# Kernel tuning notes

Hardware: AMD Instinct MI355X
Metric: run time of the kernel (lower is better)

The kernel has to match this reference:

```python
import jax, jax.numpy as jnp
import numpy as np

B, C, H, W = 4, 256, 64, 64
DIV = 4
D = C // DIV  # 64


def setup_inputs() -> dict:
    key = jax.random.key(0)
    ks = jax.random.split(key, 10)
    s = 0.05
    return {
        "x": jax.random.normal(ks[0], (B, C, H, W), dtype=jnp.float32),
        "wq": jax.random.normal(ks[1], (D, C), dtype=jnp.float32) * s,
        "bq": jax.random.normal(ks[2], (D,), dtype=jnp.float32) * s,
        "wk": jax.random.normal(ks[3], (D, C), dtype=jnp.float32) * s,
        "bk": jax.random.normal(ks[4], (D,), dtype=jnp.float32) * s,
        "wv": jax.random.normal(ks[5], (D, C), dtype=jnp.float32) * s,
        "bv": jax.random.normal(ks[6], (D,), dtype=jnp.float32) * s,
        "wsa": jax.random.normal(ks[7], (C, D), dtype=jnp.float32) * s,
        "bsa": jax.random.normal(ks[8], (C,), dtype=jnp.float32) * s,
        "gamma": jnp.zeros((1,), dtype=jnp.float32) + 0.5,
    }


def reference(x, wq, bq, wk, bk, wv, bv, wsa, bsa, gamma):
    b, c, h, w = x.shape
    hw = h * w
    xf = x.reshape(b, c, hw)  # [b, c, hw]
    # 1x1 convs == per-pixel linear maps
    q = jnp.einsum('dc,bcn->bdn', wq, xf) + bq[None, :, None]  # [b, d, hw]
    k = jnp.einsum('dc,bcn->bdn', wk, xf) + bk[None, :, None]
    v = jnp.einsum('dc,bcn->bdn', wv, xf) + bv[None, :, None]
    # attn[b, i, j] = softmax_j( q[:, :, i] . k[:, :, j] )
    scores = jnp.einsum('bdi,bdj->bij', q, k)  # [b, hw, hw]
    attn = jax.nn.softmax(scores, axis=-1)
    # sa = v @ attn^T : sa[b, d, i] = sum_j v[b, d, j] * attn[b, i, j]
    sa = jnp.einsum('bdj,bij->bdi', v, attn)  # [b, d, hw]
    out = jnp.einsum('cd,bdn->bcn', wsa, sa) + bsa[None, :, None]  # [b, c, hw]
    out = out.reshape(b, c, h, w)
    return gamma[0] * out + x
```

## Files before the change

kernel.cpp:

```cpp
#include <hip/hip_runtime.h>
#include <hip/hip_bf16.h>

typedef short short8 __attribute__((ext_vector_type(8)));
typedef float f32x4  __attribute__((ext_vector_type(4)));

static constexpr int NB  = 4;
static constexpr int NC  = 256;
static constexpr int NHW = 4096;
static constexpr int ND  = 64;
static constexpr int SPLIT = 8;
static constexpr int JITER = NHW / 64 / SPLIT;
static constexpr float SHIFT = 12.0f;

__device__ inline float bfbits2f(unsigned short u) {
    union { unsigned int i; float f; } x; x.i = ((unsigned int)u) << 16; return x.f;
}

__global__ __launch_bounds__(256) void wcvt_kernel(
    const float* __restrict__ wq, const float* __restrict__ wk,
    const float* __restrict__ wv, const float* __restrict__ wsa,
    __hip_bfloat16* __restrict__ wqkv_bf, __hip_bfloat16* __restrict__ wsa_bf)
{
    const int idx = blockIdx.x * 256 + threadIdx.x;
    if (idx < 192 * 256) {
        const int row = idx >> 8, col = idx & 255;
        const float* src = row < 64 ? wq : (row < 128 ? wk : wv);
        wqkv_bf[idx] = __float2bfloat16(src[(row & 63) * 256 + col]);
    } else {
        const int i = idx - 192 * 256;
        wsa_bf[i] = __float2bfloat16(wsa[i]);
    }
}

__global__ __launch_bounds__(512) void qkv_kernel(
    const float* __restrict__ x, const __hip_bfloat16* __restrict__ wqkv,
    const float* __restrict__ bq, const float* __restrict__ bk,
    const float* __restrict__ bv,
    __hip_bfloat16* __restrict__ qt, __hip_bfloat16* __restrict__ kt,
    __hip_bfloat16* __restrict__ vd)
{
    const int b  = blockIdx.x;
    const int n0 = blockIdx.y * 32;
    __shared__ __align__(16) __hip_bfloat16 xs[32][256];
    __shared__ __align__(16) __hip_bfloat16 vt_s[64][40];

    const int t  = threadIdx.x;
    const int tn = t & 31;
    const int cq = t >> 5;

    const float* xb = x + (size_t)b * NC * NHW + n0;
    #pragma unroll
    for (int kblk = 0; kblk < 4; ++kblk) {
        const int c0 = cq * 4 + kblk * 64;
        __hip_bfloat16 pk[4];
        #pragma unroll
        for (int j = 0; j < 4; ++j)
            pk[j] = __float2bfloat16(xb[(size_t)(c0 + j) * NHW + tn]);
        const int kk = (c0 >> 3) ^ (tn & 7);
        *(uint2*)&xs[tn][kk * 8 + (c0 & 7)] = *(uint2*)pk;
    }
    __syncthreads();

    const int w    = t >> 6;
    const int wm   = w >> 2;
    const int wn   = w & 3;
    const int lane = t & 63;
    const int c    = lane & 15;
    const int q    = lane >> 4;

    f32x4 acc[3];
    #pragma unroll
    for (int nt = 0; nt < 3; ++nt) acc[nt] = (f32x4){0.f, 0.f, 0.f, 0.f};

    const int row = wm * 16 + c;
    #pragma unroll
    for (int kc = 0; kc < 8; ++kc) {
        const int kk = (kc * 4 + q) ^ (row & 7);
        const short8 a = *(const short8*)&xs[row][kk * 8];
        #pragma unroll
        for (int nt = 0; nt < 3; ++nt) {
            const short8 bfr = *(const short8*)(wqkv
                + (size_t)(wn * 48 + nt * 16 + c) * 256 + kc * 32 + q * 8);
            acc[nt] = __builtin_amdgcn_mfma_f32_16x16x32_bf16(a, bfr, acc[nt], 0, 0, 0);
        }
    }

    #pragma unroll
    for (int nt = 0; nt < 3; ++nt) {
        const int j0   = wn * 48 + nt * 16;
        const int sel  = j0 >> 6;
        const int colr = (j0 & 63) + c;
        const float bias = (sel == 0 ? bq : (sel == 1 ? bk : bv))[colr];
        if (sel < 2) {
            __hip_bfloat16* dst = (sel == 0 ? qt : kt);
            #pragma unroll
            for (int r = 0; r < 4; ++r) {
                const int prow = wm * 16 + q * 4 + r;
                dst[((size_t)(b * NHW) + n0 + prow) * ND + colr] =
                    __float2bfloat16(acc[nt][r] + bias);
            }
        } else {
            #pragma unroll
            for (int r = 0; r < 4; ++r)
                vt_s[colr][wm * 16 + q * 4 + r] =
                    __float2bfloat16(acc[nt][r] + bias);
        }
    }
    __syncthreads();
    if (t < 256) {
        const int d = t >> 2, nc8 = (t & 3) * 8;
        *(short8*)(vd + ((size_t)(b * ND) + d) * NHW + n0 + nc8) =
            *(const short8*)&vt_s[d][nc8];
    }
}

__global__ __launch_bounds__(256, 4) void attn_kernel(
    const __hip_bfloat16* __restrict__ qt,
    const __hip_bfloat16* __restrict__ kt,
    const __hip_bfloat16* __restrict__ vd,
    __hip_bfloat16* __restrict__ O_part, float* __restrict__ l_part)
{
    const int b  = blockIdx.x;
    const int q0 = blockIdx.y * 128;
    const int s  = blockIdx.z;

    __shared__ __align__(16) __hip_bfloat16 ks [64][72];
    __shared__ __align__(16) __hip_bfloat16 vts[64][72];
    __shared__ __align__(16) __hip_bfloat16 ps [4][32][72];

    const int t    = threadIdx.x;
    const int w    = t >> 6;
    const int lane = t & 63;
    const int c    = lane & 15;
    const int q    = lane >> 4;

    short8 qf[2][2];
    #pragma unroll
    for (int mt = 0; mt < 2; ++mt)
        #pragma unroll
        for (int ch = 0; ch < 2; ++ch)
            qf[mt][ch] = *(const short8*)(qt
                + ((size_t)(b * NHW) + q0 + w * 32 + mt * 16 + c) * ND
                + ch * 32 + q * 8);

    f32x4 O[2][4];
    #pragma unroll
    for (int mt = 0; mt < 2; ++mt)
        #pragma unroll
        for (int dt = 0; dt < 4; ++dt)
            O[mt][dt] = (f32x4){0.f, 0.f, 0.f, 0.f};
    float lsum[2] = {0.f, 0.f};

    const int row_s = t >> 3;
    const int c8    = (t & 7) * 8;
    short8 kpre[2], vpre[2];
    {
        const int j0 = s * (NHW / SPLIT);
        kpre[0] = *(const short8*)(kt + ((size_t)(b * NHW) + j0 + row_s) * ND + c8);
        kpre[1] = *(const short8*)(kt + ((size_t)(b * NHW) + j0 + 32 + row_s) * ND + c8);
        vpre[0] = *(const short8*)(vd + ((size_t)(b * ND) + row_s) * NHW + j0 + c8);
        vpre[1] = *(const short8*)(vd + ((size_t)(b * ND) + 32 + row_s) * NHW + j0 + c8);
    }

    for (int it = 0; it < JITER; ++it) {
        __syncthreads();
        *(short8*)&ks [row_s     ][c8] = kpre[0];
        *(short8*)&ks [32 + row_s][c8] = kpre[1];
        *(short8*)&vts[row_s     ][c8] = vpre[0];
        *(short8*)&vts[32 + row_s][c8] = vpre[1];
        if (it + 1 < JITER) {
            const int j0 = s * (NHW / SPLIT) + (it + 1) * 64;
            kpre[0] = *(const short8*)(kt + ((size_t)(b * NHW) + j0 + row_s) * ND + c8);
            kpre[1] = *(const short8*)(kt + ((size_t)(b * NHW) + j0 + 32 + row_s) * ND + c8);
            vpre[0] = *(const short8*)(vd + ((size_t)(b * ND) + row_s) * NHW + j0 + c8);
            vpre[1] = *(const short8*)(vd + ((size_t)(b * ND) + 32 + row_s) * NHW + j0 + c8);
        }
        __syncthreads();

        #pragma unroll
        for (int jt = 0; jt < 4; ++jt) {
            const short8 kf0 = *(const short8*)&ks[jt * 16 + c][q * 8];
            const short8 kf1 = *(const short8*)&ks[jt * 16 + c][32 + q * 8];
            #pragma unroll
            for (int mt = 0; mt < 2; ++mt) {
                f32x4 acc = (f32x4){0.f, 0.f, 0.f, 0.f};
                acc = __builtin_amdgcn_mfma_f32_16x16x32_bf16(kf0, qf[mt][0], acc, 0, 0, 0);
                acc = __builtin_amdgcn_mfma_f32_16x16x32_bf16(kf1, qf[mt][1], acc, 0, 0, 0);
                __hip_bfloat16 pk[4];
                float ls = 0.f;
                #pragma unroll
                for (int r = 0; r < 4; ++r) {
                    const float p = __expf(acc[r] - SHIFT);
                    ls += p;
                    pk[r] = __float2bfloat16(p);
                }
                lsum[mt] += ls;
                *(uint2*)&ps[w][mt * 16 + c][jt * 16 + q * 4] = *(uint2*)pk;
            }
        }

        short8 af[2][2];
        #pragma unroll
        for (int mt = 0; mt < 2; ++mt) {
            af[mt][0] = *(const short8*)&ps[w][mt * 16 + c][q * 8];
            af[mt][1] = *(const short8*)&ps[w][mt * 16 + c][32 + q * 8];
        }
        #pragma unroll
        for (int dt = 0; dt < 4; ++dt) {
            const short8 vf0 = *(const short8*)&vts[dt * 16 + c][q * 8];
            const short8 vf1 = *(const short8*)&vts[dt * 16 + c][32 + q * 8];
            #pragma unroll
            for (int mt = 0; mt < 2; ++mt) {
                O[mt][dt] = __builtin_amdgcn_mfma_f32_16x16x32_bf16(af[mt][0], vf0, O[mt][dt], 0, 0, 0);
                O[mt][dt] = __builtin_amdgcn_mfma_f32_16x16x32_bf16(af[mt][1], vf1, O[mt][dt], 0, 0, 0);
            }
        }
    }

    const size_t sb = (size_t)(s * NB + b);
    #pragma unroll
    for (int mt = 0; mt < 2; ++mt) {
        float lv = lsum[mt];
        lv += __shfl_xor(lv, 16);
        lv += __shfl_xor(lv, 32);
        if (lane < 16)
            l_part[sb * NHW + q0 + w * 32 + mt * 16 + c] = lv;
    }
    #pragma unroll
    for (int mt = 0; mt < 2; ++mt)
        #pragma unroll
        for (int dt = 0; dt < 4; ++dt)
            #pragma unroll
            for (int r = 0; r < 4; ++r) {
                const int row = q0 + w * 32 + mt * 16 + q * 4 + r;
                O_part[(sb * NHW + row) * ND + dt * 16 + c] =
                    __float2bfloat16(O[mt][dt][r]);
            }
}

__global__ __launch_bounds__(256) void combine_kernel(
    const __hip_bfloat16* __restrict__ O_part, const float* __restrict__ l_part,
    __hip_bfloat16* __restrict__ sat)
{
    const int idx = blockIdx.x * 256 + threadIdx.x;
    const size_t bn = (size_t)(idx >> 4);
    const int d4 = (idx & 15) * 4;
    float num[4] = {0.f, 0.f, 0.f, 0.f};
    float den = 0.f;
    #pragma unroll
    for (int s = 0; s < SPLIT; ++s) {
        den += l_part[(size_t)s * NB * NHW + bn];
        const unsigned short* op = (const unsigned short*)(O_part
            + ((size_t)s * NB * NHW + bn) * ND + d4);
        ushort4 u = *(const ushort4*)op;
        num[0] += bfbits2f(u.x); num[1] += bfbits2f(u.y);
        num[2] += bfbits2f(u.z); num[3] += bfbits2f(u.w);
    }
    const float inv = 1.f / den;
    __hip_bfloat16 o[4];
    #pragma unroll
    for (int j = 0; j < 4; ++j) o[j] = __float2bfloat16(num[j] * inv);
    *(uint2*)(sat + bn * ND + d4) = *(uint2*)o;
}

__global__ __launch_bounds__(512) void out_kernel(
    const __hip_bfloat16* __restrict__ sat,
    const __hip_bfloat16* __restrict__ wsa_bf,
    const float* __restrict__ bsa, const float* __restrict__ g,
    const float* __restrict__ x, float* __restrict__ out)
{
    const int b  = blockIdx.x;
    const int n0 = blockIdx.y * 32;
    const int t  = threadIdx.x;
    const int w  = t >> 6;
    const int lane = t & 63;
    const int c  = lane & 15;
    const int q  = lane >> 4;

    short8 bf[2][2];
    #pragma unroll
    for (int nt = 0; nt < 2; ++nt)
        #pragma unroll
        for (int ch = 0; ch < 2; ++ch)
            bf[nt][ch] = *(const short8*)(sat
                + ((size_t)(b * NHW) + n0 + nt * 16 + c) * ND + ch * 32 + q * 8);

    short8 af[2][2];
    #pragma unroll
    for (int mt = 0; mt < 2; ++mt)
        #pragma unroll
        for (int ch = 0; ch < 2; ++ch)
            af[mt][ch] = *(const short8*)(wsa_bf
                + ((size_t)(w * 32 + mt * 16 + c)) * ND + ch * 32 + q * 8);

    f32x4 acc[2][2];
    #pragma unroll
    for (int mt = 0; mt < 2; ++mt)
        #pragma unroll
        for (int nt = 0; nt < 2; ++nt) {
            f32x4 a = (f32x4){0.f, 0.f, 0.f, 0.f};
            a = __builtin_amdgcn_mfma_f32_16x16x32_bf16(af[mt][0], bf[nt][0], a, 0, 0, 0);
            a = __builtin_amdgcn_mfma_f32_16x16x32_bf16(af[mt][1], bf[nt][1], a, 0, 0, 0);
            acc[mt][nt] = a;
        }

    const float gamma = g[0];
    #pragma unroll
    for (int mt = 0; mt < 2; ++mt) {
        float biasr[4];
        #pragma unroll
        for (int r = 0; r < 4; ++r)
            biasr[r] = bsa[w * 32 + mt * 16 + q * 4 + r];
        #pragma unroll
        for (int nt = 0; nt < 2; ++nt)
            #pragma unroll
            for (int r = 0; r < 4; ++r) {
                const int crow = w * 32 + mt * 16 + q * 4 + r;
                const size_t oi = ((size_t)(b * NC) + crow) * NHW + n0 + nt * 16 + c;
                out[oi] = gamma * (acc[mt][nt][r] + biasr[r]) + x[oi];
            }
    }
}

extern "C" void kernel_launch(void* const* d_in, const int* in_sizes, int n_in,
                              void* d_out, int out_size, void* d_ws, size_t ws_size,
                              hipStream_t stream)
{
    const float* x     = (const float*)d_in[0];
    const float* wq    = (const float*)d_in[1];
    const float* bq    = (const float*)d_in[2];
    const float* wk    = (const float*)d_in[3];
    const float* bk    = (const float*)d_in[4];
    const float* wv    = (const float*)d_in[5];
    const float* bv    = (const float*)d_in[6];
    const float* wsa   = (const float*)d_in[7];
    const float* bsa   = (const float*)d_in[8];
    const float* gamma = (const float*)d_in[9];
    float* out = (float*)d_out;

    char* p = (char*)d_ws;
    __hip_bfloat16* wqkv_bf = (__hip_bfloat16*)p; p += (size_t)128 << 10;
    __hip_bfloat16* wsa_bf  = (__hip_bfloat16*)p; p += (size_t)128 << 10;
    __hip_bfloat16* qt = (__hip_bfloat16*)p; p += (size_t)2 << 20;
    __hip_bfloat16* kt = (__hip_bfloat16*)p; p += (size_t)2 << 20;
    __hip_bfloat16* vd = (__hip_bfloat16*)p; p += (size_t)2 << 20;
    __hip_bfloat16* O_part = (__hip_bfloat16*)p; p += (size_t)16 << 20;
    float* l_part = (float*)p; p += (size_t)1 << 20;
    __hip_bfloat16* sat = (__hip_bfloat16*)p; p += (size_t)2 << 20;

    wcvt_kernel<<<dim3(256), 256, 0, stream>>>(wq, wk, wv, wsa, wqkv_bf, wsa_bf);
    qkv_kernel<<<dim3(NB, NHW / 32), 512, 0, stream>>>(
        x, wqkv_bf, bq, bk, bv, qt, kt, vd);
    attn_kernel<<<dim3(NB, NHW / 128, SPLIT), 256, 0, stream>>>(
        qt, kt, vd, O_part, l_part);
    combine_kernel<<<dim3(NB * NHW * 16 / 256), 256, 0, stream>>>(
        O_part, l_part, sat);
    out_kernel<<<dim3(NB, NHW / 32), 512, 0, stream>>>(
        sat, wsa_bf, bsa, gamma, x, out);
}
```

Baseline: 136.5 us.

## Fuse split-K combine into output projection and coalesce epilogue stores via LDS

```diff
diff --git a/kernel.cpp b/kernel.cpp
--- a/kernel.cpp
+++ b/kernel.cpp
@@ -43,6 +43,8 @@
     const int n0 = blockIdx.y * 32;
     __shared__ __align__(16) __hip_bfloat16 xs[32][256];
     __shared__ __align__(16) __hip_bfloat16 vt_s[64][40];
+    __shared__ __align__(16) __hip_bfloat16 qs [32][72];
+    __shared__ __align__(16) __hip_bfloat16 ks2[32][72];
 
     const int t  = threadIdx.x;
     const int tn = t & 31;
@@ -92,13 +94,11 @@
         const int colr = (j0 & 63) + c;
         const float bias = (sel == 0 ? bq : (sel == 1 ? bk : bv))[colr];
         if (sel < 2) {
-            __hip_bfloat16* dst = (sel == 0 ? qt : kt);
-            #pragma unroll
-            for (int r = 0; r < 4; ++r) {
-                const int prow = wm * 16 + q * 4 + r;
-                dst[((size_t)(b * NHW) + n0 + prow) * ND + colr] =
+            __hip_bfloat16 (*dst)[72] = (sel == 0 ? qs : ks2);
+            #pragma unroll
+            for (int r = 0; r < 4; ++r)
+                dst[wm * 16 + q * 4 + r][colr] =
                     __float2bfloat16(acc[nt][r] + bias);
-            }
         } else {
             #pragma unroll
             for (int r = 0; r < 4; ++r)
@@ -107,10 +107,20 @@
         }
     }
     __syncthreads();
-    if (t < 256) {
-        const int d = t >> 2, nc8 = (t & 3) * 8;
-        *(short8*)(vd + ((size_t)(b * ND) + d) * NHW + n0 + nc8) =
-            *(const short8*)&vt_s[d][nc8];
+    for (int task = t; task < 768; task += 512) {
+        const int which = task >> 8;
+        const int i = task & 255;
+        if (which == 0) {
+            const int d = i >> 2, nc8 = (i & 3) * 8;
+            *(short8*)(vd + ((size_t)(b * ND) + d) * NHW + n0 + nc8) =
+                *(const short8*)&vt_s[d][nc8];
+        } else {
+            __hip_bfloat16* dst = (which == 1) ? qt : kt;
+            const __hip_bfloat16 (*src)[72] = (which == 1) ? qs : ks2;
+            const int n = i >> 3, d8 = (i & 7) * 8;
+            *(short8*)(dst + ((size_t)(b * NHW) + n0 + n) * ND + d8) =
+                *(const short8*)&src[n][d8];
+        }
     }
 }
 
@@ -238,33 +248,8 @@
             }
 }
 
-__global__ __launch_bounds__(256) void combine_kernel(
+__global__ __launch_bounds__(512) void out_kernel(
     const __hip_bfloat16* __restrict__ O_part, const float* __restrict__ l_part,
-    __hip_bfloat16* __restrict__ sat)
-{
-    const int idx = blockIdx.x * 256 + threadIdx.x;
-    const size_t bn = (size_t)(idx >> 4);
-    const int d4 = (idx & 15) * 4;
-    float num[4] = {0.f, 0.f, 0.f, 0.f};
-    float den = 0.f;
-    #pragma unroll
-    for (int s = 0; s < SPLIT; ++s) {
-        den += l_part[(size_t)s * NB * NHW + bn];
-        const unsigned short* op = (const unsigned short*)(O_part
-            + ((size_t)s * NB * NHW + bn) * ND + d4);
-        ushort4 u = *(const ushort4*)op;
-        num[0] += bfbits2f(u.x); num[1] += bfbits2f(u.y);
-        num[2] += bfbits2f(u.z); num[3] += bfbits2f(u.w);
-    }
-    const float inv = 1.f / den;
-    __hip_bfloat16 o[4];
-    #pragma unroll
-    for (int j = 0; j < 4; ++j) o[j] = __float2bfloat16(num[j] * inv);
-    *(uint2*)(sat + bn * ND + d4) = *(uint2*)o;
-}
-
-__global__ __launch_bounds__(512) void out_kernel(
-    const __hip_bfloat16* __restrict__ sat,
     const __hip_bfloat16* __restrict__ wsa_bf,
     const float* __restrict__ bsa, const float* __restrict__ g,
     const float* __restrict__ x, float* __restrict__ out)
@@ -272,53 +257,86 @@
     const int b  = blockIdx.x;
     const int n0 = blockIdx.y * 32;
     const int t  = threadIdx.x;
-    const int w  = t >> 6;
-    const int lane = t & 63;
-    const int c  = lane & 15;
-    const int q  = lane >> 4;
-
-    short8 bf[2][2];
-    #pragma unroll
-    for (int nt = 0; nt < 2; ++nt)
-        #pragma unroll
-        for (int ch = 0; ch < 2; ++ch)
-            bf[nt][ch] = *(const short8*)(sat
-                + ((size_t)(b * NHW) + n0 + nt * 16 + c) * ND + ch * 32 + q * 8);
-
-    short8 af[2][2];
-    #pragma unroll
-    for (int mt = 0; mt < 2; ++mt)
-        #pragma unroll
-        for (int ch = 0; ch < 2; ++ch)
-            af[mt][ch] = *(const short8*)(wsa_bf
-                + ((size_t)(w * 32 + mt * 16 + c)) * ND + ch * 32 + q * 8);
-
-    f32x4 acc[2][2];
-    #pragma unroll
-    for (int mt = 0; mt < 2; ++mt)
-        #pragma unroll
-        for (int nt = 0; nt < 2; ++nt) {
-            f32x4 a = (f32x4){0.f, 0.f, 0.f, 0.f};
-            a = __builtin_amdgcn_mfma_f32_16x16x32_bf16(af[mt][0], bf[nt][0], a, 0, 0, 0);
-            a = __builtin_amdgcn_mfma_f32_16x16x32_bf16(af[mt][1], bf[nt][1], a, 0, 0, 0);
-            acc[mt][nt] = a;
-        }
+
+    __shared__ __align__(16) __hip_bfloat16 sat_s[32][72];
+    __shared__ __align__(16) float os[256][33];
+
+    {
+        const int n  = t >> 4;
+        const int d4 = (t & 15) * 4;
+        const size_t bn = (size_t)b * NHW + n0 + n;
+        float num[4] = {0.f, 0.f, 0.f, 0.f};
+        float den = 0.f;
+        #pragma unroll
+        for (int s = 0; s < SPLIT; ++s) {
+            den += l_part[(size_t)s * NB * NHW + bn];
+            const unsigned short* op = (const unsigned short*)(O_part
+                + ((size_t)s * NB * NHW + bn) * ND + d4);
+            ushort4 u = *(const ushort4*)op;
+            num[0] += bfbits2f(u.x); num[1] += bfbits2f(u.y);
+            num[2] += bfbits2f(u.z); num[3] += bfbits2f(u.w);
+        }
+        const float inv = 1.f / den;
+        __hip_bfloat16 o4[4];
+        #pragma unroll
+        for (int j = 0; j < 4; ++j) o4[j] = __float2bfloat16(num[j] * inv);
+        *(uint2*)&sat_s[n][d4] = *(uint2*)o4;
+    }
+    __syncthreads();
+
+    {
+        const int w    = t >> 6;
+        const int lane = t & 63;
+        const int c    = lane & 15;
+        const int q    = lane >> 4;
+
+        short8 bfr[2][2];
+        #pragma unroll
+        for (int nt = 0; nt < 2; ++nt)
+            #pragma unroll
+            for (int ch = 0; ch < 2; ++ch)
+                bfr[nt][ch] = *(const short8*)&sat_s[nt * 16 + c][ch * 32 + q * 8];
+
+        short8 af[2][2];
+        #pragma unroll
+        for (int mt = 0; mt < 2; ++mt)
+            #pragma unroll
+            for (int ch = 0; ch < 2; ++ch)
+                af[mt][ch] = *(const short8*)(wsa_bf
+                    + ((size_t)(w * 32 + mt * 16 + c)) * ND + ch * 32 + q * 8);
+
+        #pragma unroll
+        for (int mt = 0; mt < 2; ++mt) {
+            float biasr[4];
+            #pragma unroll
+            for (int r = 0; r < 4; ++r)
+                biasr[r] = bsa[w * 32 + mt * 16 + q * 4 + r];
+            #pragma unroll
+            for (int nt = 0; nt < 2; ++nt) {
+                f32x4 a = (f32x4){0.f, 0.f, 0.f, 0.f};
+                a = __builtin_amdgcn_mfma_f32_16x16x32_bf16(af[mt][0], bfr[nt][0], a, 0, 0, 0);
+                a = __builtin_amdgcn_mfma_f32_16x16x32_bf16(af[mt][1], bfr[nt][1], a, 0, 0, 0);
+                #pragma unroll
+                for (int r = 0; r < 4; ++r)
+                    os[w * 32 + mt * 16 + q * 4 + r][nt * 16 + c] = a[r] + biasr[r];
+            }
+        }
+    }
+    __syncthreads();
 
     const float gamma = g[0];
     #pragma unroll
-    for (int mt = 0; mt < 2; ++mt) {
-        float biasr[4];
-        #pragma unroll
-        for (int r = 0; r < 4; ++r)
-            biasr[r] = bsa[w * 32 + mt * 16 + q * 4 + r];
-        #pragma unroll
-        for (int nt = 0; nt < 2; ++nt)
-            #pragma unroll
-            for (int r = 0; r < 4; ++r) {
-                const int crow = w * 32 + mt * 16 + q * 4 + r;
-                const size_t oi = ((size_t)(b * NC) + crow) * NHW + n0 + nt * 16 + c;
-                out[oi] = gamma * (acc[mt][nt][r] + biasr[r]) + x[oi];
-            }
+    for (int pass = 0; pass < 4; ++pass) {
+        const int row = pass * 64 + (t >> 3);
+        const int nq  = (t & 7) * 4;
+        const size_t oi = ((size_t)(b * NC) + row) * NHW + n0 + nq;
+        const float4 xv = *(const float4*)(x + oi);
+        float4 ov;
+        ov.x = gamma * os[row][nq + 0] + xv.x;
+        ov.y = gamma * os[row][nq + 1] + xv.y;
+        ov.z = gamma * os[row][nq + 2] + xv.z;
+        ov.w = gamma * os[row][nq + 3] + xv.w;
+        *(float4*)(out + oi) = ov;
     }
 }
 
@@ -346,15 +364,12 @@
     __hip_bfloat16* vd = (__hip_bfloat16*)p; p += (size_t)2 << 20;
     __hip_bfloat16* O_part = (__hip_bfloat16*)p; p += (size_t)16 << 20;
     float* l_part = (float*)p; p += (size_t)1 << 20;
-    __hip_bfloat16* sat = (__hip_bfloat16*)p; p += (size_t)2 << 20;
 
     wcvt_kernel<<<dim3(256), 256, 0, stream>>>(wq, wk, wv, wsa, wqkv_bf, wsa_bf);
     qkv_kernel<<<dim3(NB, NHW / 32), 512, 0, stream>>>(
         x, wqkv_bf, bq, bk, bv, qt, kt, vd);
     attn_kernel<<<dim3(NB, NHW / 128, SPLIT), 256, 0, stream>>>(
         qt, kt, vd, O_part, l_part);
-    combine_kernel<<<dim3(NB * NHW * 16 / 256), 256, 0, stream>>>(
-        O_part, l_part, sat);
     out_kernel<<<dim3(NB, NHW / 32), 512, 0, stream>>>(
-        sat, wsa_bf, bsa, gamma, x, out);
-}
+        O_part, l_part, wsa_bf, bsa, gamma, x, out);
+}
```

After: 133.9 us. Within noise of the previous version (-1.9%).
